# Kernel tuning notes

Hardware: AMD Instinct MI355X
Metric: run time of the kernel (lower is better)

Reference implementation:

```python
import jax, jax.numpy as jnp
import numpy as np

B, NPG = 64, 512          # graphs, nodes per graph
N_TOTAL = B * NPG
LIG = 128                 # ligand nodes per graph (segment 0); rest are protein (segment 1)
BOX = 40.0                # Angstrom box for random coords -> realistic radius-graph density
INTER_CUTOFF = 10.0       # normalize_coord is identity (scale=1)
INTRA_CUTOFF = 8.0


def setup_inputs() -> dict:
    key = jax.random.key(0)
    X = jax.random.uniform(key, (N_TOTAL, 1, 3), dtype=jnp.float32) * BOX
    batch_id = jnp.repeat(jnp.arange(B, dtype=jnp.int32), NPG)
    local = jnp.tile(jnp.arange(NPG, dtype=jnp.int32), B)
    segment_id = (local >= LIG).astype(jnp.int32)
    is_global = jnp.logical_or(local == 0, local == LIG)  # one global node per segment
    return {"X": X, "batch_id": batch_id, "segment_id": segment_id, "is_global": is_global}


def _radial_edges(X, src_dst, cutoff):
    # src_dst: [E, 2] node indices; X: [N, C, 3], channel 0 holds coords
    p = X[:, 0][src_dst]                              # [E, 2, 3]
    dist = jnp.linalg.norm(p[:, 0] - p[:, 1], axis=-1)
    return src_dst[dist <= cutoff].T                  # [2, E']


def reference(X, batch_id, segment_id, is_global):
    N = batch_id.shape[0]
    nB = int(batch_id[-1]) + 1
    lengths = jax.ops.segment_sum(jnp.ones_like(batch_id), batch_id, num_segments=nB)
    max_n = int(jnp.max(lengths))
    offsets = jnp.concatenate([jnp.zeros((1,), lengths.dtype), jnp.cumsum(lengths)[:-1]])
    gni = jnp.arange(N)
    gni2lni = gni - offsets[batch_id]                 # local node index within its graph

    # Dense [N, max_n] same-batch mask via cumsum trick (O(N*max_n))
    same_bid = jnp.zeros((N, max_n), jnp.float32)
    same_bid = same_bid.at[gni, lengths[batch_id] - 1].set(1.0)
    same_bid = 1.0 - jnp.cumsum(same_bid, axis=-1)
    same_bid = jnp.concatenate([jnp.ones((N, 1), jnp.float32), same_bid[:, :-1]], axis=-1)
    same_bid = same_bid.at[gni, gni2lni].set(0.0)     # remove self edges

    row, col = jnp.nonzero(same_bid)                  # all same-graph candidate pairs
    col = col + offsets[batch_id[row]]                # local col -> global node index

    row_global = is_global[row]
    col_global = is_global[col]
    not_global = jnp.logical_not(jnp.logical_or(row_global, col_global))
    row_seg = segment_id[row]
    col_seg = segment_id[col]

    # intra-protein context edges (segment 1, within 8A)
    sel = (row_seg == col_seg) & (row_seg == 1) & not_global
    ctx_edges = _radial_edges(X, jnp.stack([row[sel], col[sel]], axis=1), INTRA_CUTOFF)

    # inter ligand-protein edges (within 10A)
    sel = (row_seg != col_seg) & not_global
    ir, ic = row[sel], col[sel]
    inter_edges = _radial_edges(X, jnp.stack([ir, ic], axis=1), INTER_CUTOFF)
    if inter_edges.shape[1] == 0:
        inter_edges = jnp.array([[ir[0], ic[0]], [ic[0], ir[0]]], dtype=inter_edges.dtype)

    reduced_inter_edge_batchid = batch_id[inter_edges[0][inter_edges[0] < inter_edges[1]]]
    reduced_inter_edge_offsets = offsets[reduced_inter_edge_batchid]

    # global<->same-segment edges and global<->global edges appended to context
    sel = (row_seg == col_seg) & jnp.logical_not(not_global)
    global_normal = jnp.stack([row[sel], col[sel]])
    sel = row_global & col_global
    global_global = jnp.stack([row[sel], col[sel]])
    ctx_edges = jnp.concatenate([ctx_edges, global_normal, global_global], axis=1)

    return ctx_edges, inter_edges, reduced_inter_edge_batchid, reduced_inter_edge_offsets
```

## Files before the change

### kernel.cpp

```cpp
#include <hip/hip_runtime.h>

#define NB 64
#define NPG 512
#define LIG 128
#define NBLK 1024
#define RPB 32
#define THREADS 512

__device__ __forceinline__ float dist2(float dx, float dy, float dz) {
    return __fadd_rn(__fadd_rn(__fmul_rn(dx, dx), __fmul_rn(dy, dy)), __fmul_rn(dz, dz));
}
#define T10 __uint_as_float(0x42C80001u)
#define T8  __uint_as_float(0x42800001u)

#define F21 0x1FFFFFull

__device__ __forceinline__ unsigned long long pk_triple(unsigned long long v, int j) {
    unsigned long long ci = v & F21;
    unsigned long long cc = (v >> 21) & F21;
    unsigned long long red = (j < 4) ? ci : 0ull;
    return (cc << 42) | (ci << 21) | red;
}

__global__ __launch_bounds__(THREADS, 8) void fused_kernel(const float* __restrict__ X,
                                                           unsigned long long* __restrict__ pk,
                                                           int* __restrict__ out) {
    __shared__ float s[NPG * 3];
    __shared__ unsigned long long smask[RPB * 8];
    __shared__ int rc[RPB], ri[RPB];
    __shared__ int sc[RPB], si[RPB];
    __shared__ unsigned long long sblkb, stot;
    __shared__ int sint;

    const int b = blockIdx.x;
    const int g = b >> 4;
    const int h = b & 15;
    const int t = threadIdx.x;
    const int lane = t & 63;
    const int w = t >> 6;

    if (t < 384) ((float4*)s)[t] = ((const float4*)X)[g * 384 + t];
    if (t < RPB * 8) smask[t] = 0ull;
    __syncthreads();

    float cx[8], cy[8], cz[8];
#pragma unroll
    for (int k = 0; k < 8; ++k) {
        const int c = k * 64 + lane;
        cx[k] = s[3 * c]; cy[k] = s[3 * c + 1]; cz[k] = s[3 * c + 2];
    }

#pragma unroll
    for (int j = 0; j < 4; ++j) {
        const int lr = w * 4 + j;
        const int r = h * 32 + lr;
        const float px = s[3 * r], py = s[3 * r + 1], pz = s[3 * r + 2];
        int cc = 0, ci = 0;
        if (h < 4) {
            if (r != 0) {
                unsigned long long mm[6];
#pragma unroll
                for (int k = 2; k < 8; ++k) {
                    unsigned long long m =
                        __ballot(dist2(px - cx[k], py - cy[k], pz - cz[k]) <= T10);
                    if (k == 2) m &= ~1ull;
                    mm[k - 2] = m;
                    ci += __popcll(m);
                }
                if (lane == 0) {
#pragma unroll
                    for (int k = 0; k < 6; ++k) smask[lr * 8 + 2 + k] = mm[k];
                }
            }
        } else if (r != LIG) {
            unsigned long long mm[8];
#pragma unroll
            for (int k = 0; k < 2; ++k) {
                unsigned long long m =
                    __ballot(dist2(px - cx[k], py - cy[k], pz - cz[k]) <= T10);
                if (k == 0) m &= ~1ull;
                mm[k] = m;
                ci += __popcll(m);
            }
            const int kr = r >> 6;
            const unsigned long long selfbit = 1ull << (r & 63);
#pragma unroll
            for (int k = 2; k < 8; ++k) {
                unsigned long long m =
                    __ballot(dist2(px - cx[k], py - cy[k], pz - cz[k]) <= T8);
                if (k == 2) m &= ~1ull;
                if (k == kr) m &= ~selfbit;
                mm[k] = m;
                cc += __popcll(m);
            }
            if (lane == 0) {
#pragma unroll
                for (int k = 0; k < 8; ++k) smask[lr * 8 + k] = mm[k];
            }
        }
        if (lane == 0) { rc[lr] = cc; ri[lr] = ci; }
    }
    __syncthreads();

    if (w == 0) {
        int c = (lane < RPB) ? rc[lane] : 0;
        int ii = (lane < RPB) ? ri[lane] : 0;
#pragma unroll
        for (int off = 32; off >= 1; off >>= 1) {
            c += __shfl_down(c, off, 64);
            ii += __shfl_down(ii, off, 64);
        }
        if (lane == 0) {
            const unsigned long long q = (1ull << 63) |
                ((unsigned long long)(unsigned)c << 21) | (unsigned long long)(unsigned)ii;
            __hip_atomic_store(&pk[b], q, __ATOMIC_RELAXED, __HIP_MEMORY_SCOPE_AGENT);
        }
        const int base = lane * 16;
        unsigned long long sum = 0;
#pragma unroll
        for (int j = 0; j < 16; ++j) {
            unsigned long long v =
                __hip_atomic_load(&pk[base + j], __ATOMIC_RELAXED, __HIP_MEMORY_SCOPE_AGENT);
            int guard = 0;
            while (!(v >> 63) && ++guard < (1 << 20)) {
                __builtin_amdgcn_s_sleep(8);
                v = __hip_atomic_load(&pk[base + j], __ATOMIC_RELAXED, __HIP_MEMORY_SCOPE_AGENT);
            }
            sum += pk_triple(v, j);
        }
        unsigned long long incl = sum;
#pragma unroll
        for (int off = 1; off < 64; off <<= 1) {
            unsigned long long n = __shfl_up(incl, off, 64);
            if (lane >= off) incl += n;
        }
        if (lane == (b >> 4)) {
            unsigned long long e = incl - sum;
            const int idx = b & 15;
            for (int jj = 0; jj < idx; ++jj) {
                unsigned long long v =
                    __hip_atomic_load(&pk[base + jj], __ATOMIC_RELAXED, __HIP_MEMORY_SCOPE_AGENT);
                e += pk_triple(v, jj);
            }
            sblkb = e;
        }
        if (lane == 63) stot = incl;
    }
    __syncthreads();

    const int blkb0 = (int)((sblkb >> 42) & F21);
    const int blkb1 = (int)((sblkb >> 21) & F21);
    const int blkb2 = (int)(sblkb & F21);
    const int Eci = (int)((stot >> 42) & F21);
    const int Ei  = (int)((stot >> 21) & F21);
    const int Er  = (int)(stot & F21);

    if (t < RPB) {
        const int mc = rc[t];
        const int mi = ri[t];
        int ic = mc, ii = mi;
#pragma unroll
        for (int off = 1; off < 32; off <<= 1) {
            int a0 = __shfl_up(ic, off, 64);
            int a1 = __shfl_up(ii, off, 64);
            if (lane >= off) { ic += a0; ii += a1; }
        }
        sc[t] = blkb0 + ic - mc;
        si[t] = blkb1 + ii - mi;
        if (t == RPB - 1) sint = ii;
    }
    __syncthreads();

    const unsigned long long lmask = (1ull << lane) - 1ull;
    const int gn = g * NPG;
    const int Ectx = Eci + NB * 1020 + NB * 2;

    int* ctx_src   = out;
    int* ctx_dst   = out + Ectx;
    int* inter_src = out + 2 * Ectx;
    int* inter_dst = inter_src + Ei;
    int* red_bid   = out + 2 * Ectx + 2 * Ei;
    int* red_off   = red_bid + Er;

    for (int j = 0; j < 4; ++j) {
        const int lr = w * 4 + j;
        const int r = h * 32 + lr;
        const int row = gn + r;

        unsigned long long m[8];
#pragma unroll
        for (int k = 0; k < 8; ++k) m[k] = smask[lr * 8 + k];

        if (h < 4) {
            if (r == 0) {
                for (int k = 0; k < 2; ++k) {
                    const int c = k * 64 + lane;
                    if (c >= 1 && c < LIG) {
                        const int pos = Eci + g * 1020 + (c - 1);
                        ctx_src[pos] = row; ctx_dst[pos] = gn + c;
                    }
                }
                if (lane == 0) {
                    const int pos = Eci + NB * 1020 + g * 2;
                    ctx_src[pos] = row; ctx_dst[pos] = gn + LIG;
                }
            } else {
                int ib = si[lr];
#pragma unroll
                for (int k = 2; k < 8; ++k) {
                    if (m[k]) {
                        if ((m[k] >> lane) & 1ull) {
                            const int c = k * 64 + lane;
                            const int p = __popcll(m[k] & lmask);
                            inter_src[ib + p] = row; inter_dst[ib + p] = gn + c;
                        }
                        ib += __popcll(m[k]);
                    }
                }
                if (lane == 0) {
                    const int pos = Eci + g * 1020 + (LIG - 1) + (r - 1);
                    ctx_src[pos] = row; ctx_dst[pos] = gn;
                }
            }
        } else {
            if (r == LIG) {
                for (int k = 2; k < 8; ++k) {
                    const int c = k * 64 + lane;
                    if (c > LIG) {
                        const int pos = Eci + g * 1020 + 2 * (LIG - 1) + (c - LIG - 1);
                        ctx_src[pos] = row; ctx_dst[pos] = gn + c;
                    }
                }
                if (lane == 0) {
                    const int pos = Eci + NB * 1020 + g * 2 + 1;
                    ctx_src[pos] = row; ctx_dst[pos] = gn;
                }
            } else {
                int ib = si[lr];
#pragma unroll
                for (int k = 0; k < 2; ++k) {
                    if (m[k]) {
                        if ((m[k] >> lane) & 1ull) {
                            const int c = k * 64 + lane;
                            const int pos = ib + __popcll(m[k] & lmask);
                            inter_src[pos] = row; inter_dst[pos] = gn + c;
                        }
                        ib += __popcll(m[k]);
                    }
                }
                int cb = sc[lr];
#pragma unroll
                for (int k = 2; k < 8; ++k) {
                    if (m[k]) {
                        if ((m[k] >> lane) & 1ull) {
                            const int c = k * 64 + lane;
                            const int pos = cb + __popcll(m[k] & lmask);
                            ctx_src[pos] = row; ctx_dst[pos] = gn + c;
                        }
                        cb += __popcll(m[k]);
                    }
                }
                if (lane == 0) {
                    const int pos = Eci + g * 1020 + 2 * (LIG - 1) + (NPG - LIG - 1) + (r - LIG - 1);
                    ctx_src[pos] = row; ctx_dst[pos] = gn + LIG;
                }
            }
        }
    }

    if (h < 4) {
        const int rb0 = blkb2;
        const int n = sint;
        for (int i = t; i < n; i += THREADS) {
            red_bid[rb0 + i] = g;
            red_off[rb0 + i] = gn;
        }
    }
}

extern "C" void kernel_launch(void* const* d_in, const int* in_sizes, int n_in,
                              void* d_out, int out_size, void* d_ws, size_t ws_size,
                              hipStream_t stream) {
    (void)in_sizes; (void)n_in; (void)out_size; (void)ws_size;
    const float* X = (const float*)d_in[0];
    unsigned long long* pk = (unsigned long long*)d_ws;
    int* out = (int*)d_out;

    hipMemsetAsync(pk, 0, NBLK * sizeof(unsigned long long), stream);
    fused_kernel<<<NBLK, THREADS, 0, stream>>>(X, pk, out);
}
```

Before: 85.84 us.

## Centralize grid-wide prefix scan in block 0 and broadcast per-block offsets

```diff
diff --git a/kernel.cpp b/kernel.cpp
--- a/kernel.cpp
+++ b/kernel.cpp
@@ -13,7 +13,12 @@
 #define T10 __uint_as_float(0x42C80001u)
 #define T8  __uint_as_float(0x42800001u)
 
-#define F21 0x1FFFFFull
+#define F21  0x1FFFFFull
+#define FLG  (1ull << 63)
+
+__device__ __forceinline__ unsigned long long rmw_read(unsigned long long* p) {
+    return __hip_atomic_fetch_add(p, 0ull, __ATOMIC_RELAXED, __HIP_MEMORY_SCOPE_AGENT);
+}
 
 __device__ __forceinline__ unsigned long long pk_triple(unsigned long long v, int j) {
     unsigned long long ci = v & F21;
@@ -24,6 +29,7 @@
 
 __global__ __launch_bounds__(THREADS, 8) void fused_kernel(const float* __restrict__ X,
                                                            unsigned long long* __restrict__ pk,
+                                                           unsigned long long* __restrict__ rel,
                                                            int* __restrict__ out) {
     __shared__ float s[NPG * 3];
     __shared__ unsigned long long smask[RPB * 8];
@@ -111,40 +117,58 @@
             ii += __shfl_down(ii, off, 64);
         }
         if (lane == 0) {
-            const unsigned long long q = (1ull << 63) |
+            const unsigned long long q = FLG |
                 ((unsigned long long)(unsigned)c << 21) | (unsigned long long)(unsigned)ii;
             __hip_atomic_store(&pk[b], q, __ATOMIC_RELAXED, __HIP_MEMORY_SCOPE_AGENT);
         }
-        const int base = lane * 16;
-        unsigned long long sum = 0;
-#pragma unroll
-        for (int j = 0; j < 16; ++j) {
-            unsigned long long v =
-                __hip_atomic_load(&pk[base + j], __ATOMIC_RELAXED, __HIP_MEMORY_SCOPE_AGENT);
+
+        if (b == 0) {
+            const int base = lane * 16;
+            unsigned long long sum = 0;
             int guard = 0;
-            while (!(v >> 63) && ++guard < (1 << 20)) {
+            for (;;) {
+                unsigned long long conj = ~0ull;
+                sum = 0;
+#pragma unroll
+                for (int j = 0; j < 16; ++j) {
+                    const unsigned long long v = rmw_read(&pk[base + j]);
+                    conj &= v;
+                    sum += pk_triple(v, j);
+                }
+                if (__all((int)(conj >> 63)) || ++guard >= (1 << 15)) break;
+                __builtin_amdgcn_s_sleep(4);
+            }
+            unsigned long long incl = sum;
+#pragma unroll
+            for (int off = 1; off < 64; off <<= 1) {
+                unsigned long long n = __shfl_up(incl, off, 64);
+                if (lane >= off) incl += n;
+            }
+            const unsigned long long excl = incl - sum;
+            const unsigned long long tots = __shfl(incl, 63);
+            unsigned long long running = excl;
+#pragma unroll
+            for (int j = 0; j < 16; ++j) {
+                const unsigned long long v = rmw_read(&pk[base + j]);
+                __hip_atomic_store(&rel[2 * (base + j)], FLG | running,
+                                   __ATOMIC_RELAXED, __HIP_MEMORY_SCOPE_AGENT);
+                __hip_atomic_store(&rel[2 * (base + j) + 1], FLG | tots,
+                                   __ATOMIC_RELAXED, __HIP_MEMORY_SCOPE_AGENT);
+                running += pk_triple(v, j);
+            }
+            if (lane == 0) { sblkb = 0ull; stot = tots; }
+        } else {
+            unsigned long long vv = 0ull;
+            int guard = 0;
+            for (;;) {
+                if (lane < 2) vv = rmw_read(&rel[2 * b + lane]);
+                const int flagged = (lane < 2) ? (int)(vv >> 63) : 1;
+                if (__all(flagged) || ++guard >= (1 << 15)) break;
                 __builtin_amdgcn_s_sleep(8);
-                v = __hip_atomic_load(&pk[base + j], __ATOMIC_RELAXED, __HIP_MEMORY_SCOPE_AGENT);
-            }
-            sum += pk_triple(v, j);
-        }
-        unsigned long long incl = sum;
-#pragma unroll
-        for (int off = 1; off < 64; off <<= 1) {
-            unsigned long long n = __shfl_up(incl, off, 64);
-            if (lane >= off) incl += n;
-        }
-        if (lane == (b >> 4)) {
-            unsigned long long e = incl - sum;
-            const int idx = b & 15;
-            for (int jj = 0; jj < idx; ++jj) {
-                unsigned long long v =
-                    __hip_atomic_load(&pk[base + jj], __ATOMIC_RELAXED, __HIP_MEMORY_SCOPE_AGENT);
-                e += pk_triple(v, jj);
-            }
-            sblkb = e;
-        }
-        if (lane == 63) stot = incl;
+            }
+            if (lane == 0) sblkb = vv & ~FLG;
+            if (lane == 1) stot  = vv & ~FLG;
+        }
     }
     __syncthreads();
 
@@ -283,9 +307,10 @@
                               hipStream_t stream) {
     (void)in_sizes; (void)n_in; (void)out_size; (void)ws_size;
     const float* X = (const float*)d_in[0];
-    unsigned long long* pk = (unsigned long long*)d_ws;
+    unsigned long long* pk  = (unsigned long long*)d_ws;
+    unsigned long long* rel = pk + NBLK;
     int* out = (int*)d_out;
 
-    hipMemsetAsync(pk, 0, NBLK * sizeof(unsigned long long), stream);
-    fused_kernel<<<NBLK, THREADS, 0, stream>>>(X, pk, out);
-}
+    hipMemsetAsync(d_ws, 0, (NBLK + 2 * NBLK) * sizeof(unsigned long long), stream);
+    fused_kernel<<<NBLK, THREADS, 0, stream>>>(X, pk, rel, out);
+}
```

New measurement: 89.07 us. 3.8% more time.
